# Performance work log

Measured on AMD Instinct MI355X. Metric: run time of the kernel, lower is better.

## Reference

```python
import jax, jax.numpy as jnp
import numpy as np

DIM = 256
HEADS = 8
DIM_HEAD = 32
INNER = HEADS * DIM_HEAD
K_NEIGHBORS = 16
TEMPERATURE = 1.0
SCALE = DIM_HEAD ** (-0.5)
BATCH = 512
N_FEATURES = 32


def setup_inputs() -> dict:
    key = jax.random.key(0)
    ks = jax.random.split(key, 6)
    s = 0.02
    return {
        "x": jax.random.normal(ks[0], (BATCH, N_FEATURES, DIM), dtype=jnp.float32),
        "W_qkv": jax.random.normal(ks[1], (DIM, 3 * INNER), dtype=jnp.float32) * s,
        "W_out": jax.random.normal(ks[2], (INNER, DIM), dtype=jnp.float32) * s,
        "b_out": jnp.zeros((DIM,), dtype=jnp.float32),
        "W_repr": jax.random.normal(ks[3], (DIM, DIM), dtype=jnp.float32) * s,
        "b_repr": jnp.zeros((DIM,), dtype=jnp.float32),
    }


def reference(x, W_qkv, W_out, b_out, W_repr, b_repr):
    B, n, d = x.shape
    # A. sample representations: mean over features + linear proj
    reprs = jnp.mean(x, axis=1) @ W_repr + b_repr  # [B, dim]
    # B. kNN graph via cosine similarity
    normed = reprs / jnp.linalg.norm(reprs, axis=-1, keepdims=True)
    sim_mat = (normed @ normed.T) / TEMPERATURE  # [B, B]
    k_actual = min(K_NEIGHBORS + 1, B)
    _, knn_idx = jax.lax.top_k(sim_mat, k_actual)  # [B, k+1]
    # C. attention mask: 0 for self+neighbors, -inf elsewhere
    neg_inf = jnp.float32(-jnp.inf)
    mask = jnp.full((B, B), neg_inf, dtype=jnp.float32)
    mask = mask.at[jnp.arange(B)[:, None], knn_idx].set(0.0)  # [B, B]
    # D. masked cross-sample attention (vectorized over all features/heads)
    qkv = x @ W_qkv  # [B, n, 3*inner]
    q, k, v = jnp.split(qkv, 3, axis=-1)
    def to_bhnd(t):
        return t.reshape(B, n, HEADS, DIM_HEAD).transpose(0, 2, 1, 3)  # b h n d
    q, k, v = to_bhnd(q), to_bhnd(k), to_bhnd(v)
    # per-feature cross-sample scores: [n, b, h, B]
    sim = jnp.einsum('bhnd,Bhnd->nbhB', q, k) * SCALE
    sim = sim + mask[None, :, None, :]
    attn = jax.nn.softmax(sim, axis=-1)
    out = jnp.einsum('nbhB,Bhnd->bnhd', attn, v)  # [b, n, h, d]
    out = out.reshape(B, n, INNER)
    return out @ W_out + b_out
```

## Files before the change

### kernel.cpp

```cpp
#include <hip/hip_runtime.h>
#include <math.h>

#define DIMX 256
#define NFEAT 32
#define BATCH 512
#define HEADS 8
#define DHEAD 32
#define KNN 17
#define QKV_W 768
#define SCALE_F 0.17677669529663687f

typedef unsigned int uint;
typedef unsigned short ushort_t;
typedef __attribute__((ext_vector_type(8))) short short8_t;
typedef __attribute__((ext_vector_type(4))) float float4_t;

__device__ inline float bf_lo(uint u) { return __uint_as_float(u << 16); }
__device__ inline float bf_hi(uint u) { return __uint_as_float(u & 0xffff0000u); }
__device__ inline ushort_t f2bf(float f) {
  uint u = __float_as_uint(f);
  return (ushort_t)((u + 0x7fffu + ((u >> 16) & 1u)) >> 16);
}
__device__ inline void gload16(const ushort_t* g, ushort_t* l) {
  __builtin_amdgcn_global_load_lds(
      (const __attribute__((address_space(1))) void*)g,
      (__attribute__((address_space(3))) void*)l, 16, 0, 0);
}

__global__ void repr_kernel(const float* __restrict__ x, const float* __restrict__ W_repr,
                            const float* __restrict__ b_repr, float* __restrict__ normed,
                            ushort_t* __restrict__ xbf) {
  int b = blockIdx.x, t = threadIdx.x;
  __shared__ float mean_s[DIMX];
  __shared__ float red[DIMX];
  float s = 0.f;
#pragma unroll
  for (int n = 0; n < NFEAT; ++n) {
    float v = x[(size_t)(b*NFEAT+n)*DIMX + t];
    s += v;
    xbf[(size_t)(b*NFEAT+n)*DIMX + t] = f2bf(v);
  }
  mean_s[t] = s * (1.0f/NFEAT);
  __syncthreads();
  float acc = b_repr[t];
  for (int d = 0; d < DIMX; ++d) acc += mean_s[d] * W_repr[d*DIMX + t];
  red[t] = acc*acc;
  __syncthreads();
  for (int off = 128; off > 0; off >>= 1) {
    if (t < off) red[t] += red[t+off];
    __syncthreads();
  }
  normed[b*DIMX + t] = acc / sqrtf(red[0]);
}

__global__ __launch_bounds__(256, 4) void sim_gemm(const float* __restrict__ normed,
                                                   float* __restrict__ sims) {
  __shared__ float As[32][68];
  __shared__ float Bs[32][68];
  int t = threadIdx.x;
  int i0 = blockIdx.x * 32, j0 = blockIdx.y * 32;
  int tx = t & 15, ty = t >> 4;
  float acc00 = 0.f, acc01 = 0.f, acc10 = 0.f, acc11 = 0.f;
  for (int k0 = 0; k0 < DIMX; k0 += 64) {
#pragma unroll
    for (int c = t; c < 512; c += 256) {
      int r = c >> 4, cc = (c & 15) * 4;
      *(float4*)&As[r][cc] = *(const float4*)&normed[(size_t)(i0 + r)*DIMX + k0 + cc];
      *(float4*)&Bs[r][cc] = *(const float4*)&normed[(size_t)(j0 + r)*DIMX + k0 + cc];
    }
    __syncthreads();
#pragma unroll 16
    for (int kk = 0; kk < 64; ++kk) {
      float a0 = As[ty*2][kk],   a1 = As[ty*2+1][kk];
      float b0 = Bs[tx*2][kk],   b1 = Bs[tx*2+1][kk];
      acc00 += a0*b0; acc01 += a0*b1; acc10 += a1*b0; acc11 += a1*b1;
    }
    __syncthreads();
  }
  sims[(size_t)(i0+ty*2  )*BATCH + j0+tx*2  ] = acc00;
  sims[(size_t)(i0+ty*2  )*BATCH + j0+tx*2+1] = acc01;
  sims[(size_t)(i0+ty*2+1)*BATCH + j0+tx*2  ] = acc10;
  sims[(size_t)(i0+ty*2+1)*BATCH + j0+tx*2+1] = acc11;
}

__global__ __launch_bounds__(256, 8) void topk_rank(const float* __restrict__ sims,
                                                    int* __restrict__ knn) {
  int i = blockIdx.x, t = threadIdx.x;
  __shared__ float row[BATCH];
  row[t]       = sims[(size_t)i*BATCH + t];
  row[t + 256] = sims[(size_t)i*BATCH + t + 256];
  __syncthreads();
  float v1 = row[t], v2 = row[t + 256];
  int i1 = t, i2 = t + 256;
  int r1 = 0, r2 = 0;
  const float4* r4 = (const float4*)row;
#pragma unroll 8
  for (int c = 0; c < BATCH/4; ++c) {
    float4 q = r4[c];
    int base = c * 4;
    r1 += (q.x > v1 || (q.x == v1 && base+0 < i1));
    r1 += (q.y > v1 || (q.y == v1 && base+1 < i1));
    r1 += (q.z > v1 || (q.z == v1 && base+2 < i1));
    r1 += (q.w > v1 || (q.w == v1 && base+3 < i1));
    r2 += (q.x > v2 || (q.x == v2 && base+0 < i2));
    r2 += (q.y > v2 || (q.y == v2 && base+1 < i2));
    r2 += (q.z > v2 || (q.z == v2 && base+2 < i2));
    r2 += (q.w > v2 || (q.w == v2 && base+3 < i2));
  }
  if (r1 < KNN) knn[i*32 + r1] = i1;
  if (r2 < KNN) knn[i*32 + r2] = i2;
}

__global__ void prep_kernel(const float* __restrict__ Wq, const float* __restrict__ Wo,
                            ushort_t* __restrict__ wqT, ushort_t* __restrict__ woT) {
  int bid = blockIdx.x, t = threadIdx.x;
  if (bid < QKV_W) {
    wqT[(size_t)bid*DIMX + t] = f2bf(Wq[(size_t)t*QKV_W + bid]);
  } else {
    int c = bid - QKV_W;
    woT[(size_t)c*DIMX + t] = f2bf(Wo[(size_t)t*DIMX + c]);
  }
}

template<bool OUTF32>
__global__ __launch_bounds__(256, 2) void mfma_gemm(
    const ushort_t* __restrict__ A, const ushort_t* __restrict__ Bt,
    void* __restrict__ Cout, const float* __restrict__ bias, int M, int N, int K) {
  __shared__ ushort_t As[128][64];
  __shared__ ushort_t Bs[128][64];
  int t = threadIdx.x, l = t & 63, w = t >> 6;
  int wr = w >> 1, wc = w & 1;
  int row0 = blockIdx.x * 128, col0 = blockIdx.y * 128;
  int srcRow = l >> 3;
  int srcCol = (l & 7) * 8;
  float4_t acc[4][4] = {};
  for (int k0 = 0; k0 < K; k0 += 64) {
#pragma unroll
    for (int i = 0; i < 4; ++i) {
      int ar = w*32 + i*8;
      gload16(&A [(size_t)(row0+ar+srcRow)*K + k0 + srcCol], &As[ar][0]);
      gload16(&Bt[(size_t)(col0+ar+srcRow)*K + k0 + srcCol], &Bs[ar][0]);
    }
    __syncthreads();
#pragma unroll
    for (int ks = 0; ks < 2; ++ks) {
      int kk = ks*32 + (l >> 4)*8;
      short8_t a[4], b[4];
#pragma unroll
      for (int m = 0; m < 4; ++m) a[m] = *(short8_t*)&As[wr*64 + m*16 + (l & 15)][kk];
#pragma unroll
      for (int n = 0; n < 4; ++n) b[n] = *(short8_t*)&Bs[wc*64 + n*16 + (l & 15)][kk];
#pragma unroll
      for (int m = 0; m < 4; ++m)
#pragma unroll
        for (int n = 0; n < 4; ++n)
          acc[m][n] = __builtin_amdgcn_mfma_f32_16x16x32_bf16(a[m], b[n], acc[m][n], 0, 0, 0);
    }
    __syncthreads();
  }
  int crow = (l >> 4) * 4, ccol = l & 15;
#pragma unroll
  for (int m = 0; m < 4; ++m)
#pragma unroll
    for (int n = 0; n < 4; ++n) {
      int col = col0 + wc*64 + n*16 + ccol;
#pragma unroll
      for (int r = 0; r < 4; ++r) {
        int row = row0 + wr*64 + m*16 + crow + r;
        if (OUTF32) ((float*)Cout)[(size_t)row*N + col] = acc[m][n][r] + bias[col];
        else        ((ushort_t*)Cout)[(size_t)row*N + col] = f2bf(acc[m][n][r]);
      }
    }
}

#define NF_BLK 8
__global__ __launch_bounds__(256, 8) void attn_kernel(
    const ushort_t* __restrict__ qkv, const int* __restrict__ knn,
    ushort_t* __restrict__ attn_out) {
  int b = blockIdx.x, g = blockIdx.y, t = threadIdx.x;
  int n0 = g * NF_BLK;
  __shared__ float sc_s[KNN][HEADS];
  __shared__ uint  v_lds[KNN][DIMX/2];
  __shared__ int idxs[KNN];
  if (t < KNN) idxs[t] = knn[b*32 + t];
  __syncthreads();

  for (int nn = 0; nn < NF_BLK; ++nn) {
    int n = n0 + nn;
    if (t < KNN*HEADS) {
      int j = t >> 3, h = t & 7;
      const uint4* qp = (const uint4*)&qkv[(size_t)(b*NFEAT + n)*QKV_W + h*DHEAD];
      const uint4* kp = (const uint4*)&qkv[(size_t)(idxs[j]*NFEAT + n)*QKV_W + 256 + h*DHEAD];
      float s = 0.f;
#pragma unroll
      for (int i = 0; i < 4; ++i) {
        uint4 qv = qp[i], kv = kp[i];
        s += bf_lo(qv.x)*bf_lo(kv.x) + bf_hi(qv.x)*bf_hi(kv.x)
           + bf_lo(qv.y)*bf_lo(kv.y) + bf_hi(qv.y)*bf_hi(kv.y)
           + bf_lo(qv.z)*bf_lo(kv.z) + bf_hi(qv.z)*bf_hi(kv.z)
           + bf_lo(qv.w)*bf_lo(kv.w) + bf_hi(qv.w)*bf_hi(kv.w);
      }
      sc_s[j][h] = s * SCALE_F;
    } else {
      for (int idx = t - 136; idx < KNN*32; idx += 120) {
        int row = idx >> 5, col = idx & 31;
        uint4 wv = ((const uint4*)&qkv[(size_t)(idxs[row]*NFEAT + n)*QKV_W + 512])[col];
        ((uint4*)&v_lds[row][0])[col] = wv;
      }
    }
    __syncthreads();
    if (t < HEADS) {
      float m = -INFINITY;
#pragma unroll
      for (int j = 0; j < KNN; ++j) m = fmaxf(m, sc_s[j][t]);
      float sum = 0.f;
      float e[KNN];
#pragma unroll
      for (int j = 0; j < KNN; ++j) { e[j] = __expf(sc_s[j][t] - m); sum += e[j]; }
      float inv = 1.0f / sum;
#pragma unroll
      for (int j = 0; j < KNN; ++j) sc_s[j][t] = e[j] * inv;
    }
    __syncthreads();
    {
      int h = t >> 5;
      int word = t >> 1;
      bool hi = (t & 1);
      float acc = 0.f;
#pragma unroll
      for (int j = 0; j < KNN; ++j) {
        uint wv = v_lds[j][word];
        float v = hi ? bf_hi(wv) : bf_lo(wv);
        acc += sc_s[j][h] * v;
      }
      attn_out[(size_t)(b*NFEAT + n)*DIMX + t] = f2bf(acc);
    }
    __syncthreads();
  }
}

extern "C" void kernel_launch(void* const* d_in, const int* in_sizes, int n_in,
                              void* d_out, int out_size, void* d_ws, size_t ws_size,
                              hipStream_t stream) {
  const float* x      = (const float*)d_in[0];
  const float* W_qkv  = (const float*)d_in[1];
  const float* W_out  = (const float*)d_in[2];
  const float* b_out  = (const float*)d_in[3];
  const float* W_repr = (const float*)d_in[4];
  const float* b_repr = (const float*)d_in[5];
  float* out = (float*)d_out;

  ushort_t* qkv      = (ushort_t*)d_ws;
  ushort_t* xbf      = qkv + (size_t)16384*QKV_W;
  ushort_t* wqT      = xbf + (size_t)16384*DIMX;
  ushort_t* woT      = wqT + (size_t)QKV_W*DIMX;
  ushort_t* attn_out = woT + (size_t)DIMX*DIMX;
  float*    normed   = (float*)(attn_out + (size_t)16384*DIMX);
  float*    sims     = normed + (size_t)BATCH*DIMX;
  int*      knn      = (int*)(sims + (size_t)BATCH*BATCH);

  repr_kernel<<<BATCH, 256, 0, stream>>>(x, W_repr, b_repr, normed, xbf);
  sim_gemm<<<dim3(BATCH/32, BATCH/32), 256, 0, stream>>>(normed, sims);
  topk_rank<<<BATCH, 256, 0, stream>>>(sims, knn);
  prep_kernel<<<QKV_W + DIMX, 256, 0, stream>>>(W_qkv, W_out, wqT, woT);
  mfma_gemm<false><<<dim3(16384/128, QKV_W/128), 256, 0, stream>>>(
      xbf, wqT, qkv, nullptr, 16384, QKV_W, DIMX);
  attn_kernel<<<dim3(BATCH, NFEAT/NF_BLK), 256, 0, stream>>>(qkv, knn, attn_out);
  mfma_gemm<true><<<dim3(16384/128, DIMX/128), 256, 0, stream>>>(
      attn_out, woT, out, b_out, 16384, DIMX, DIMX);
}
```

Before: 111.0 us.

## Double-buffer GEMM LDS tiles, tile weight transpose, and pair features in attention

The MFMA GEMM now double-buffers its A/B tiles in LDS, so the async global-to-LDS loads for the next K tile are issued before the current tile's MFMAs run. The weight prep kernel becomes a 64x64 LDS-tiled transpose with vectorized bf16 stores instead of strided per-element reads. The attention kernel processes two features per iteration with all threads busy, reads V straight from global instead of staging it in LDS, and computes softmax per thread. Costs are doubled GEMM LDS (which can lower occupancy) and recomputed exps in attention.

```diff
diff --git a/kernel.cpp b/kernel.cpp
--- a/kernel.cpp
+++ b/kernel.cpp
@@ -111,45 +111,72 @@
   if (r2 < KNN) knn[i*32 + r2] = i2;
 }
 
-__global__ void prep_kernel(const float* __restrict__ Wq, const float* __restrict__ Wo,
-                            ushort_t* __restrict__ wqT, ushort_t* __restrict__ woT) {
+__global__ __launch_bounds__(256, 4) void prep_kernel(
+    const float* __restrict__ Wq, const float* __restrict__ Wo,
+    ushort_t* __restrict__ wqT, ushort_t* __restrict__ woT) {
   int bid = blockIdx.x, t = threadIdx.x;
-  if (bid < QKV_W) {
-    wqT[(size_t)bid*DIMX + t] = f2bf(Wq[(size_t)t*QKV_W + bid]);
-  } else {
-    int c = bid - QKV_W;
-    woT[(size_t)c*DIMX + t] = f2bf(Wo[(size_t)t*DIMX + c]);
-  }
+  const float* W; ushort_t* WT; int NN, tx, ty;
+  if (bid < 48) { W = Wq; WT = wqT; NN = QKV_W; tx = bid % 12; ty = bid / 12; }
+  else { int b2 = bid - 48; W = Wo; WT = woT; NN = DIMX; tx = b2 % 4; ty = b2 / 4; }
+  __shared__ float tile[64][65];
+#pragma unroll
+  for (int i = 0; i < 4; ++i) {
+    int c = t + 256*i;
+    int r = c >> 4, c4 = (c & 15) * 4;
+    *(float4*)&tile[r][c4] = *(const float4*)&W[(size_t)(ty*64 + r)*NN + tx*64 + c4];
+  }
+  __syncthreads();
+  int rr = t >> 2, cc0 = (t & 3) * 16;
+  uint ow[8];
+#pragma unroll
+  for (int k = 0; k < 8; ++k)
+    ow[k] = (uint)f2bf(tile[cc0 + 2*k][rr]) | ((uint)f2bf(tile[cc0 + 2*k + 1][rr]) << 16);
+  uint4 o0 = {ow[0], ow[1], ow[2], ow[3]};
+  uint4 o1 = {ow[4], ow[5], ow[6], ow[7]};
+  size_t obase = (size_t)(tx*64 + rr)*DIMX + ty*64 + cc0;
+  *(uint4*)&WT[obase]     = o0;
+  *(uint4*)&WT[obase + 8] = o1;
 }
 
 template<bool OUTF32>
 __global__ __launch_bounds__(256, 2) void mfma_gemm(
     const ushort_t* __restrict__ A, const ushort_t* __restrict__ Bt,
     void* __restrict__ Cout, const float* __restrict__ bias, int M, int N, int K) {
-  __shared__ ushort_t As[128][64];
-  __shared__ ushort_t Bs[128][64];
+  __shared__ ushort_t As[2][128][64];
+  __shared__ ushort_t Bs[2][128][64];
   int t = threadIdx.x, l = t & 63, w = t >> 6;
   int wr = w >> 1, wc = w & 1;
   int row0 = blockIdx.x * 128, col0 = blockIdx.y * 128;
   int srcRow = l >> 3;
   int srcCol = (l & 7) * 8;
   float4_t acc[4][4] = {};
-  for (int k0 = 0; k0 < K; k0 += 64) {
-#pragma unroll
-    for (int i = 0; i < 4; ++i) {
-      int ar = w*32 + i*8;
-      gload16(&A [(size_t)(row0+ar+srcRow)*K + k0 + srcCol], &As[ar][0]);
-      gload16(&Bt[(size_t)(col0+ar+srcRow)*K + k0 + srcCol], &Bs[ar][0]);
-    }
-    __syncthreads();
+  int nkt = K >> 6;
+#pragma unroll
+  for (int i = 0; i < 4; ++i) {
+    int ar = w*32 + i*8;
+    gload16(&A [(size_t)(row0+ar+srcRow)*K + srcCol], &As[0][ar][0]);
+    gload16(&Bt[(size_t)(col0+ar+srcRow)*K + srcCol], &Bs[0][ar][0]);
+  }
+  __syncthreads();
+  int cur = 0;
+  for (int kt = 0; kt < nkt; ++kt) {
+    if (kt + 1 < nkt) {
+      int k1 = (kt + 1) << 6;
+#pragma unroll
+      for (int i = 0; i < 4; ++i) {
+        int ar = w*32 + i*8;
+        gload16(&A [(size_t)(row0+ar+srcRow)*K + k1 + srcCol], &As[cur^1][ar][0]);
+        gload16(&Bt[(size_t)(col0+ar+srcRow)*K + k1 + srcCol], &Bs[cur^1][ar][0]);
+      }
+    }
 #pragma unroll
     for (int ks = 0; ks < 2; ++ks) {
       int kk = ks*32 + (l >> 4)*8;
       short8_t a[4], b[4];
 #pragma unroll
-      for (int m = 0; m < 4; ++m) a[m] = *(short8_t*)&As[wr*64 + m*16 + (l & 15)][kk];
-#pragma unroll
-      for (int n = 0; n < 4; ++n) b[n] = *(short8_t*)&Bs[wc*64 + n*16 + (l & 15)][kk];
+      for (int m = 0; m < 4; ++m) a[m] = *(short8_t*)&As[cur][wr*64 + m*16 + (l & 15)][kk];
+#pragma unroll
+      for (int n = 0; n < 4; ++n) b[n] = *(short8_t*)&Bs[cur][wc*64 + n*16 + (l & 15)][kk];
 #pragma unroll
       for (int m = 0; m < 4; ++m)
 #pragma unroll
@@ -157,6 +184,7 @@
           acc[m][n] = __builtin_amdgcn_mfma_f32_16x16x32_bf16(a[m], b[n], acc[m][n], 0, 0, 0);
     }
     __syncthreads();
+    cur ^= 1;
   }
   int crow = (l >> 4) * 4, ccol = l & 15;
 #pragma unroll
@@ -179,18 +207,19 @@
     ushort_t* __restrict__ attn_out) {
   int b = blockIdx.x, g = blockIdx.y, t = threadIdx.x;
   int n0 = g * NF_BLK;
-  __shared__ float sc_s[KNN][HEADS];
-  __shared__ uint  v_lds[KNN][DIMX/2];
+  __shared__ float sc_s[2][KNN][HEADS];
   __shared__ int idxs[KNN];
   if (t < KNN) idxs[t] = knn[b*32 + t];
   __syncthreads();
 
-  for (int nn = 0; nn < NF_BLK; ++nn) {
-    int n = n0 + nn;
-    if (t < KNN*HEADS) {
-      int j = t >> 3, h = t & 7;
-      const uint4* qp = (const uint4*)&qkv[(size_t)(b*NFEAT + n)*QKV_W + h*DHEAD];
-      const uint4* kp = (const uint4*)&qkv[(size_t)(idxs[j]*NFEAT + n)*QKV_W + 256 + h*DHEAD];
+  for (int np = 0; np < NF_BLK; np += 2) {
+    int n = n0 + np;
+    for (int job = t; job < 2*KNN*HEADS; job += 256) {
+      int f = (job >= KNN*HEADS) ? 1 : 0;
+      int r = job - f*KNN*HEADS;
+      int j = r >> 3, h = r & 7;
+      const uint4* qp = (const uint4*)&qkv[(size_t)(b*NFEAT + n + f)*QKV_W + h*DHEAD];
+      const uint4* kp = (const uint4*)&qkv[(size_t)(idxs[j]*NFEAT + n + f)*QKV_W + 256 + h*DHEAD];
       float s = 0.f;
 #pragma unroll
       for (int i = 0; i < 4; ++i) {
@@ -200,40 +229,28 @@
            + bf_lo(qv.z)*bf_lo(kv.z) + bf_hi(qv.z)*bf_hi(kv.z)
            + bf_lo(qv.w)*bf_lo(kv.w) + bf_hi(qv.w)*bf_hi(kv.w);
       }
-      sc_s[j][h] = s * SCALE_F;
-    } else {
-      for (int idx = t - 136; idx < KNN*32; idx += 120) {
-        int row = idx >> 5, col = idx & 31;
-        uint4 wv = ((const uint4*)&qkv[(size_t)(idxs[row]*NFEAT + n)*QKV_W + 512])[col];
-        ((uint4*)&v_lds[row][0])[col] = wv;
-      }
-    }
-    __syncthreads();
-    if (t < HEADS) {
+      sc_s[f][j][h] = s * SCALE_F;
+    }
+    __syncthreads();
+    {
+      int f = t >> 7, p = t & 127, h = p >> 4;
       float m = -INFINITY;
 #pragma unroll
-      for (int j = 0; j < KNN; ++j) m = fmaxf(m, sc_s[j][t]);
+      for (int j = 0; j < KNN; ++j) m = fmaxf(m, sc_s[f][j][h]);
       float sum = 0.f;
-      float e[KNN];
-#pragma unroll
-      for (int j = 0; j < KNN; ++j) { e[j] = __expf(sc_s[j][t] - m); sum += e[j]; }
+#pragma unroll
+      for (int j = 0; j < KNN; ++j) sum += __expf(sc_s[f][j][h] - m);
       float inv = 1.0f / sum;
-#pragma unroll
-      for (int j = 0; j < KNN; ++j) sc_s[j][t] = e[j] * inv;
-    }
-    __syncthreads();
-    {
-      int h = t >> 5;
-      int word = t >> 1;
-      bool hi = (t & 1);
-      float acc = 0.f;
+      float alo = 0.f, ahi = 0.f;
 #pragma unroll
       for (int j = 0; j < KNN; ++j) {
-        uint wv = v_lds[j][word];
-        float v = hi ? bf_hi(wv) : bf_lo(wv);
-        acc += sc_s[j][h] * v;
-      }
-      attn_out[(size_t)(b*NFEAT + n)*DIMX + t] = f2bf(acc);
+        float pw = __expf(sc_s[f][j][h] - m);
+        uint wv = *(const uint*)&qkv[(size_t)(idxs[j]*NFEAT + n + f)*QKV_W + 512 + p*2];
+        alo += pw * bf_lo(wv);
+        ahi += pw * bf_hi(wv);
+      }
+      *(uint*)&attn_out[(size_t)(b*NFEAT + n + f)*DIMX + p*2] =
+          (uint)f2bf(alo * inv) | ((uint)f2bf(ahi * inv) << 16);
     }
     __syncthreads();
   }
@@ -262,7 +279,7 @@
   repr_kernel<<<BATCH, 256, 0, stream>>>(x, W_repr, b_repr, normed, xbf);
   sim_gemm<<<dim3(BATCH/32, BATCH/32), 256, 0, stream>>>(normed, sims);
   topk_rank<<<BATCH, 256, 0, stream>>>(sims, knn);
-  prep_kernel<<<QKV_W + DIMX, 256, 0, stream>>>(W_qkv, W_out, wqT, woT);
+  prep_kernel<<<64, 256, 0, stream>>>(W_qkv, W_out, wqT, woT);
   mfma_gemm<false><<<dim3(16384/128, QKV_W/128), 256, 0, stream>>>(
       xbf, wqT, qkv, nullptr, 16384, QKV_W, DIMX);
   attn_kernel<<<dim3(BATCH, NFEAT/NF_BLK), 256, 0, stream>>>(qkv, knn, attn_out);
```

Measured after the change: 103.8 us. -6.5%, faster.
